# Optimization experiments

Measured on AMD Instinct MI355X. Metric: run time of the kernel, lower is better.

The kernel has to match this reference:

```python
import jax, jax.numpy as jnp
from jax import lax
import numpy as np

K = 3
PAD = (K - 1) // 2
EPS = 1e-5


def setup_inputs() -> dict:
    key = jax.random.key(0)
    k0, k1, k2, k3 = jax.random.split(key, 4)
    B, C, O, H, W = 8, 128, 128, 64, 64
    x = jax.random.normal(k0, (B, C, H, W), jnp.float32)
    bn_gamma = jnp.ones((C,), jnp.float32)
    bn_beta = jnp.zeros((C,), jnp.float32)
    bn_mean = jnp.zeros((C,), jnp.float32)
    bn_var = jnp.ones((C,), jnp.float32)
    # small offset-conv weights -> realistic sub-pixel offsets
    w_off = jax.random.normal(k1, (2 * K * K, C, K, K), jnp.float32) * 0.01
    b_off = jnp.zeros((2 * K * K,), jnp.float32)
    w_dconv = jax.random.normal(k2, (O, C, K, K), jnp.float32) * (1.0 / np.sqrt(C * K * K))
    b_dconv = jax.random.normal(k3, (O,), jnp.float32) * 0.01
    return dict(x=x, bn_gamma=bn_gamma, bn_beta=bn_beta, bn_mean=bn_mean,
                bn_var=bn_var, w_off=w_off, b_off=b_off,
                w_dconv=w_dconv, b_dconv=b_dconv)


def _conv2d(x, w, b):
    y = lax.conv_general_dilated(
        x, w, window_strides=(1, 1), padding=[(PAD, PAD), (PAD, PAD)],
        dimension_numbers=('NCHW', 'OIHW', 'NCHW'))
    return y + b[None, :, None, None]


def _deform_conv2d(x, offsets, w, b):
    # torchvision DeformConv2d semantics (deform_groups=1, groups=1, stride=1)
    B, C, H, W = x.shape
    KK = K * K
    off = offsets.reshape(B, KK, 2, H, W)  # (dy, dx) per kernel tap
    dy, dx = off[:, :, 0], off[:, :, 1]    # [B,KK,H,W]
    kh = (jnp.arange(KK) // K).astype(x.dtype)
    kw = (jnp.arange(KK) % K).astype(x.dtype)
    # sampling positions: p0 + pk - pad + offset
    py = dy + jnp.arange(H, dtype=x.dtype)[None, None, :, None] + (kh - PAD)[None, :, None, None]
    px = dx + jnp.arange(W, dtype=x.dtype)[None, None, None, :] + (kw - PAD)[None, :, None, None]
    y0 = jnp.floor(py)
    x0 = jnp.floor(px)
    wy = py - y0
    wx = px - x0
    y0i = y0.astype(jnp.int32)
    x0i = x0.astype(jnp.int32)
    xflat = x.reshape(B, C, H * W)

    def gather(yi, xi):
        valid = (yi >= 0) & (yi < H) & (xi >= 0) & (xi < W)
        idx = jnp.clip(yi, 0, H - 1) * W + jnp.clip(xi, 0, W - 1)  # [B,KK,H,W]
        vals = jax.vmap(lambda xf, ii: xf[:, ii])(xflat, idx)      # [B,C,KK,H,W]
        return vals * valid[:, None].astype(x.dtype)

    # bilinear sample with implicit zero padding outside the image
    v = (((1 - wy) * (1 - wx))[:, None] * gather(y0i, x0i)
         + ((1 - wy) * wx)[:, None] * gather(y0i, x0i + 1)
         + (wy * (1 - wx))[:, None] * gather(y0i + 1, x0i)
         + (wy * wx)[:, None] * gather(y0i + 1, x0i + 1))  # [B,C,KK,H,W]
    out = jnp.einsum('bckhw,ock->bohw', v, w.reshape(w.shape[0], C, KK))
    return out + b[None, :, None, None]


def reference(x, bn_gamma, bn_beta, bn_mean, bn_var, w_off, b_off, w_dconv, b_dconv):
    # BN (inference form) + ReLU
    inv = bn_gamma * lax.rsqrt(bn_var + EPS)
    h = jnp.maximum((x - bn_mean[None, :, None, None]) * inv[None, :, None, None]
                    + bn_beta[None, :, None, None], 0.0)
    offsets = _conv2d(h, w_off, b_off)          # [B, 2*K*K, H, W]
    return _deform_conv2d(h, offsets, w_dconv, b_dconv)
```

## Files before the change

kernel.cpp:

```cpp
#include <hip/hip_runtime.h>

#define BB 8
#define CC 128
#define OO 128
#define HH 64
#define WW 64
#define HW (HH*WW)

typedef __attribute__((ext_vector_type(8))) __bf16 bf16x8;
typedef __attribute__((ext_vector_type(4))) __bf16 bf16x4;
typedef __attribute__((ext_vector_type(4))) float  f32x4;

__global__ __launch_bounds__(256) void transform_weights(
    const float* __restrict__ w_dconv,
    const float* __restrict__ w_off,
    __bf16* __restrict__ wt_bf,
    __bf16* __restrict__ w_off_b)
{
    int idx = blockIdx.x * 256 + threadIdx.x;
    if (idx < 9 * 128 * 128) {
        int c  = idx & 127;
        int o  = (idx >> 7) & 127;
        int kk = idx >> 14;
        wt_bf[idx] = (__bf16)w_dconv[(o * 128 + c) * 9 + kk];
    }
    if (idx < 9 * 32 * 128) {
        int c  = idx & 127;
        int o  = (idx >> 7) & 31;
        int kk = idx >> 12;
        float v = (o < 18) ? w_off[o * 1152 + c * 9 + kk] : 0.f;
        w_off_b[idx] = (__bf16)v;
    }
}

__global__ __launch_bounds__(256) void bn_relu_nhwc(
    const float* __restrict__ x,
    const float* __restrict__ gamma, const float* __restrict__ beta,
    const float* __restrict__ mean,  const float* __restrict__ var,
    __bf16* __restrict__ h)
{
    __shared__ float inv_s[128], bb_s[128];
    __shared__ __bf16 tile[64 * 130];
    int blk = blockIdx.x;
    int b = blk & 7, y = blk >> 3;
    int tid = threadIdx.x;

    if (tid < 128) {
        float iv = gamma[tid] * rsqrtf(var[tid] + 1e-5f);
        inv_s[tid] = iv;
        bb_s[tid]  = beta[tid] - mean[tid] * iv;
    }
    __syncthreads();

    const float* xb = x + (size_t)b * CC * HW + (size_t)y * WW;
    #pragma unroll
    for (int i = 0; i < 8; ++i) {
        int idx = i * 256 + tid;
        int c = idx >> 4, x4 = idx & 15;
        float4 v = *(const float4*)(xb + (size_t)c * HW + x4 * 4);
        float iv = inv_s[c], bb = bb_s[c];
        tile[(x4 * 4 + 0) * 130 + c] = (__bf16)fmaxf(v.x * iv + bb, 0.f);
        tile[(x4 * 4 + 1) * 130 + c] = (__bf16)fmaxf(v.y * iv + bb, 0.f);
        tile[(x4 * 4 + 2) * 130 + c] = (__bf16)fmaxf(v.z * iv + bb, 0.f);
        tile[(x4 * 4 + 3) * 130 + c] = (__bf16)fmaxf(v.w * iv + bb, 0.f);
    }
    __syncthreads();

    __bf16* hb = h + ((size_t)b * HW + (size_t)y * WW) * CC;
    #pragma unroll
    for (int i = 0; i < 2; ++i) {
        int idx = i * 256 + tid;
        int xx = idx >> 3, c16 = idx & 7;
        const uint* src = (const uint*)&tile[xx * 130 + c16 * 16];
        uint r0 = src[0], r1 = src[1], r2 = src[2], r3 = src[3];
        uint r4 = src[4], r5 = src[5], r6 = src[6], r7 = src[7];
        uint* dst = (uint*)(hb + (size_t)xx * CC + c16 * 16);
        *(uint4*)dst       = (uint4){r0, r1, r2, r3};
        *(uint4*)(dst + 4) = (uint4){r4, r5, r6, r7};
    }
}

__global__ __launch_bounds__(256) void offset_mfma(
    const __bf16* __restrict__ h,
    const __bf16* __restrict__ w_off_b,
    const float* __restrict__ b_off,
    float* __restrict__ offs)
{
    __shared__ __align__(16) __bf16 at[64 * 136];
    __shared__ __align__(16) __bf16 bt[32 * 136];
    int blk = blockIdx.x;
    int b = blk & 7, y = blk >> 3;
    int tid = threadIdx.x;
    int lane = tid & 63;
    int wv  = __builtin_amdgcn_readfirstlane(tid >> 6);
    int l15 = lane & 15, quad = lane >> 4;

    const __bf16* hb = h + (size_t)b * HW * CC;

    f32x4 acc[2];
    acc[0] = (f32x4){0.f, 0.f, 0.f, 0.f};
    acc[1] = (f32x4){0.f, 0.f, 0.f, 0.f};

    for (int kk = 0; kk < 9; ++kk) {
        int dy = kk / 3 - 1, dx = kk % 3 - 1;
        int yy = y + dy;
        bool yok = (yy >= 0) && (yy < HH);
        __syncthreads();
        #pragma unroll
        for (int i = 0; i < 4; ++i) {
            int idx = i * 256 + tid;
            int xx = idx >> 4, c8 = idx & 15;
            int xs = xx + dx;
            uint4 v = (uint4){0u, 0u, 0u, 0u};
            if (yok && xs >= 0 && xs < WW)
                v = *(const uint4*)(hb + ((size_t)yy * WW + xs) * CC + c8 * 8);
            *(uint4*)&at[xx * 136 + c8 * 8] = v;
        }
        const __bf16* wsrc = w_off_b + (size_t)kk * 32 * 128;
        #pragma unroll
        for (int i = 0; i < 2; ++i) {
            int idx = i * 256 + tid;
            int o = idx >> 4, c8 = idx & 15;
            *(uint4*)&bt[o * 136 + c8 * 8] = *(const uint4*)(wsrc + o * 128 + c8 * 8);
        }
        __syncthreads();
        #pragma unroll
        for (int ks = 0; ks < 4; ++ks) {
            int kb = ks * 32 + quad * 8;
            bf16x8 a  = *(const bf16x8*)&at[(wv * 16 + l15) * 136 + kb];
            bf16x8 b0 = *(const bf16x8*)&bt[l15 * 136 + kb];
            bf16x8 b1 = *(const bf16x8*)&bt[(16 + l15) * 136 + kb];
            acc[0] = __builtin_amdgcn_mfma_f32_16x16x32_bf16(a, b0, acc[0], 0, 0, 0);
            acc[1] = __builtin_amdgcn_mfma_f32_16x16x32_bf16(a, b1, acc[1], 0, 0, 0);
        }
    }

    size_t ob = (size_t)b * 18 * HW + (size_t)y * WW;
    #pragma unroll
    for (int nt = 0; nt < 2; ++nt) {
        int oc = nt * 16 + l15;
        if (oc < 18) {
            float bias = b_off[oc];
            #pragma unroll
            for (int r = 0; r < 4; ++r) {
                int xx = wv * 16 + quad * 4 + r;
                offs[ob + (size_t)oc * HW + xx] = acc[nt][r] + bias;
            }
        }
    }
}

__global__ __launch_bounds__(256, 2) void deform_conv_mfma(
    const __bf16* __restrict__ h,
    const float* __restrict__ offs,
    const __bf16* __restrict__ wt,
    const float* __restrict__ b_dconv,
    float* __restrict__ out)
{
    __shared__ float pw[576 * 4];
    __shared__ int   pidx[576 * 4];
    __shared__ __align__(16) __bf16 vt[64 * 136];
    __shared__ __align__(16) __bf16 wl[128 * 136];

    int blk = blockIdx.x;
    int b = blk & 7, y = blk >> 3;
    int tid = threadIdx.x;

    const __bf16* hb = h + (size_t)b * HW * CC;
    size_t offbase = (size_t)b * 18 * HW + (size_t)y * WW;

    for (int e = tid; e < 576; e += 256) {
        int kk = e >> 6, xx = e & 63;
        float dy = offs[offbase + (size_t)(2 * kk) * HW + xx];
        float dx = offs[offbase + (size_t)(2 * kk + 1) * HW + xx];
        float py = dy + (float)y + (float)(kk / 3 - 1);
        float px = dx + (float)xx + (float)(kk % 3 - 1);
        float fy = floorf(py), fx = floorf(px);
        int y0 = (int)fy, x0 = (int)fx;
        float wy = py - fy, wx = px - fx;
        int y1 = y0 + 1, x1 = x0 + 1;
        bool vy0 = (y0 >= 0) && (y0 < HH);
        bool vy1 = (y1 >= 0) && (y1 < HH);
        bool vx0 = (x0 >= 0) && (x0 < WW);
        bool vx1 = (x1 >= 0) && (x1 < WW);
        int yc0 = min(max(y0, 0), HH - 1), yc1 = min(max(y1, 0), HH - 1);
        int xc0 = min(max(x0, 0), WW - 1), xc1 = min(max(x1, 0), WW - 1);
        pw[e * 4 + 0] = (vy0 && vx0) ? (1.f - wy) * (1.f - wx) : 0.f;
        pw[e * 4 + 1] = (vy0 && vx1) ? (1.f - wy) * wx         : 0.f;
        pw[e * 4 + 2] = (vy1 && vx0) ? wy * (1.f - wx)         : 0.f;
        pw[e * 4 + 3] = (vy1 && vx1) ? wy * wx                 : 0.f;
        pidx[e * 4 + 0] = (yc0 * WW + xc0) * CC;
        pidx[e * 4 + 1] = (yc0 * WW + xc1) * CC;
        pidx[e * 4 + 2] = (yc1 * WW + xc0) * CC;
        pidx[e * 4 + 3] = (yc1 * WW + xc1) * CC;
    }

    int lane = tid & 63;
    int wv   = __builtin_amdgcn_readfirstlane(tid >> 6);
    int l15  = lane & 15, quad = lane >> 4;
    int cl   = tid & 31, xh = tid >> 5;

    f32x4 acc[4][2];
    #pragma unroll
    for (int mt = 0; mt < 4; ++mt)
        #pragma unroll
        for (int nt = 0; nt < 2; ++nt)
            acc[mt][nt] = (f32x4){0.f, 0.f, 0.f, 0.f};

    for (int kk = 0; kk < 9; ++kk) {
        __syncthreads();
        const uint4* wsrc = (const uint4*)(wt + (size_t)kk * OO * CC);
        #pragma unroll
        for (int j = 0; j < 8; ++j) {
            int idx = j * 256 + tid;
            int cs = idx & 15, o = idx >> 4;
            *(uint4*)&wl[o * 136 + cs * 8] = wsrc[idx];
        }
        #pragma unroll
        for (int j = 0; j < 8; ++j) {
            int xx = xh * 8 + j;
            int e = (kk << 6) + xx;
            float w0 = pw[e * 4 + 0], w1 = pw[e * 4 + 1];
            float w2 = pw[e * 4 + 2], w3 = pw[e * 4 + 3];
            bf16x4 t0 = *(const bf16x4*)(hb + pidx[e * 4 + 0] + cl * 4);
            bf16x4 t1 = *(const bf16x4*)(hb + pidx[e * 4 + 1] + cl * 4);
            bf16x4 t2 = *(const bf16x4*)(hb + pidx[e * 4 + 2] + cl * 4);
            bf16x4 t3 = *(const bf16x4*)(hb + pidx[e * 4 + 3] + cl * 4);
            float rx = w0 * (float)t0[0] + w1 * (float)t1[0] + w2 * (float)t2[0] + w3 * (float)t3[0];
            float ry = w0 * (float)t0[1] + w1 * (float)t1[1] + w2 * (float)t2[1] + w3 * (float)t3[1];
            float rz = w0 * (float)t0[2] + w1 * (float)t1[2] + w2 * (float)t2[2] + w3 * (float)t3[2];
            float rw = w0 * (float)t0[3] + w1 * (float)t1[3] + w2 * (float)t2[3] + w3 * (float)t3[3];
            bf16x4 pk = {(__bf16)rx, (__bf16)ry, (__bf16)rz, (__bf16)rw};
            *(bf16x4*)&vt[xx * 136 + cl * 4] = pk;
        }
        __syncthreads();
        #pragma unroll
        for (int ks = 0; ks < 4; ++ks) {
            int kb = ks * 32 + quad * 8;
            bf16x8 a0 = *(const bf16x8*)&vt[(0 * 16 + l15) * 136 + kb];
            bf16x8 a1 = *(const bf16x8*)&vt[(1 * 16 + l15) * 136 + kb];
            bf16x8 a2 = *(const bf16x8*)&vt[(2 * 16 + l15) * 136 + kb];
            bf16x8 a3 = *(const bf16x8*)&vt[(3 * 16 + l15) * 136 + kb];
            bf16x8 b0 = *(const bf16x8*)&wl[(wv * 32 + l15) * 136 + kb];
            bf16x8 b1 = *(const bf16x8*)&wl[(wv * 32 + 16 + l15) * 136 + kb];
            acc[0][0] = __builtin_amdgcn_mfma_f32_16x16x32_bf16(a0, b0, acc[0][0], 0, 0, 0);
            acc[1][0] = __builtin_amdgcn_mfma_f32_16x16x32_bf16(a1, b0, acc[1][0], 0, 0, 0);
            acc[2][0] = __builtin_amdgcn_mfma_f32_16x16x32_bf16(a2, b0, acc[2][0], 0, 0, 0);
            acc[3][0] = __builtin_amdgcn_mfma_f32_16x16x32_bf16(a3, b0, acc[3][0], 0, 0, 0);
            acc[0][1] = __builtin_amdgcn_mfma_f32_16x16x32_bf16(a0, b1, acc[0][1], 0, 0, 0);
            acc[1][1] = __builtin_amdgcn_mfma_f32_16x16x32_bf16(a1, b1, acc[1][1], 0, 0, 0);
            acc[2][1] = __builtin_amdgcn_mfma_f32_16x16x32_bf16(a2, b1, acc[2][1], 0, 0, 0);
            acc[3][1] = __builtin_amdgcn_mfma_f32_16x16x32_bf16(a3, b1, acc[3][1], 0, 0, 0);
        }
    }

    size_t ob = (size_t)b * OO * HW + (size_t)y * WW;
    #pragma unroll
    for (int nt = 0; nt < 2; ++nt) {
        int o = wv * 32 + nt * 16 + l15;
        float bias = b_dconv[o];
        #pragma unroll
        for (int mt = 0; mt < 4; ++mt) {
            int xb = mt * 16 + quad * 4;
            float4 r;
            r.x = acc[mt][nt][0] + bias;
            r.y = acc[mt][nt][1] + bias;
            r.z = acc[mt][nt][2] + bias;
            r.w = acc[mt][nt][3] + bias;
            *(float4*)&out[ob + (size_t)o * HW + xb] = r;
        }
    }
}

extern "C" void kernel_launch(void* const* d_in, const int* in_sizes, int n_in,
                              void* d_out, int out_size, void* d_ws, size_t ws_size,
                              hipStream_t stream)
{
    const float* x       = (const float*)d_in[0];
    const float* gamma   = (const float*)d_in[1];
    const float* beta    = (const float*)d_in[2];
    const float* mean    = (const float*)d_in[3];
    const float* var     = (const float*)d_in[4];
    const float* w_off   = (const float*)d_in[5];
    const float* b_off   = (const float*)d_in[6];
    const float* w_dconv = (const float*)d_in[7];
    const float* b_dconv = (const float*)d_in[8];
    float* out = (float*)d_out;

    char* ws = (char*)d_ws;
    __bf16* h_bf    = (__bf16*)ws;
    float*  offs    = (float*)(ws + 8388608);
    __bf16* wt_bf   = (__bf16*)(ws + 10747904);
    __bf16* w_off_b = (__bf16*)(ws + 11042816);

    transform_weights<<<576, 256, 0, stream>>>(w_dconv, w_off, wt_bf, w_off_b);
    bn_relu_nhwc<<<512, 256, 0, stream>>>(x, gamma, beta, mean, var, h_bf);
    offset_mfma<<<512, 256, 0, stream>>>(h_bf, w_off_b, b_off, offs);
    deform_conv_mfma<<<512, 256, 0, stream>>>(h_bf, offs, wt_bf, b_dconv, out);
}
```

Measured before the change: 135.0 us.

## Fuse offset conv into deform conv kernel and read weights directly from global

Merges the offset-convolution kernel into the deformable-conv kernel, so each block computes its row's offsets in shared memory and no longer round-trips them through global memory or pays a separate launch. The shared-memory weight staging (wl and bt) is dropped, and MFMA B operands are loaded straight from global memory (L2/L1). This cuts LDS use enough to allow 4 blocks per CU. The cost is uncoalesced, per-wave repeated global weight loads inside the MFMA loop, which may add latency.

```diff
diff --git a/kernel.cpp b/kernel.cpp
--- a/kernel.cpp
+++ b/kernel.cpp
@@ -80,26 +80,32 @@
     }
 }
 
-__global__ __launch_bounds__(256) void offset_mfma(
+__global__ __launch_bounds__(256, 4) void fused_offset_deform(
     const __bf16* __restrict__ h,
     const __bf16* __restrict__ w_off_b,
     const float* __restrict__ b_off,
-    float* __restrict__ offs)
-{
-    __shared__ __align__(16) __bf16 at[64 * 136];
-    __shared__ __align__(16) __bf16 bt[32 * 136];
+    const __bf16* __restrict__ wt,
+    const float* __restrict__ b_dconv,
+    float* __restrict__ out)
+{
+    __shared__ float pw[576 * 4];
+    __shared__ int   pidx[576 * 4];
+    __shared__ __align__(16) __bf16 vt[64 * 136];
+    __shared__ float offs_s[18 * 65];
+
     int blk = blockIdx.x;
     int b = blk & 7, y = blk >> 3;
     int tid = threadIdx.x;
     int lane = tid & 63;
-    int wv  = __builtin_amdgcn_readfirstlane(tid >> 6);
-    int l15 = lane & 15, quad = lane >> 4;
+    int wv   = __builtin_amdgcn_readfirstlane(tid >> 6);
+    int l15  = lane & 15, quad = lane >> 4;
+    int cl   = tid & 31, xh = tid >> 5;
 
     const __bf16* hb = h + (size_t)b * HW * CC;
 
-    f32x4 acc[2];
-    acc[0] = (f32x4){0.f, 0.f, 0.f, 0.f};
-    acc[1] = (f32x4){0.f, 0.f, 0.f, 0.f};
+    f32x4 oacc[2];
+    oacc[0] = (f32x4){0.f, 0.f, 0.f, 0.f};
+    oacc[1] = (f32x4){0.f, 0.f, 0.f, 0.f};
 
     for (int kk = 0; kk < 9; ++kk) {
         int dy = kk / 3 - 1, dx = kk % 3 - 1;
@@ -114,28 +120,20 @@
             uint4 v = (uint4){0u, 0u, 0u, 0u};
             if (yok && xs >= 0 && xs < WW)
                 v = *(const uint4*)(hb + ((size_t)yy * WW + xs) * CC + c8 * 8);
-            *(uint4*)&at[xx * 136 + c8 * 8] = v;
-        }
-        const __bf16* wsrc = w_off_b + (size_t)kk * 32 * 128;
-        #pragma unroll
-        for (int i = 0; i < 2; ++i) {
-            int idx = i * 256 + tid;
-            int o = idx >> 4, c8 = idx & 15;
-            *(uint4*)&bt[o * 136 + c8 * 8] = *(const uint4*)(wsrc + o * 128 + c8 * 8);
-        }
-        __syncthreads();
+            *(uint4*)&vt[xx * 136 + c8 * 8] = v;
+        }
+        __syncthreads();
+        const __bf16* wk = w_off_b + (size_t)kk * 32 * 128;
         #pragma unroll
         for (int ks = 0; ks < 4; ++ks) {
             int kb = ks * 32 + quad * 8;
-            bf16x8 a  = *(const bf16x8*)&at[(wv * 16 + l15) * 136 + kb];
-            bf16x8 b0 = *(const bf16x8*)&bt[l15 * 136 + kb];
-            bf16x8 b1 = *(const bf16x8*)&bt[(16 + l15) * 136 + kb];
-            acc[0] = __builtin_amdgcn_mfma_f32_16x16x32_bf16(a, b0, acc[0], 0, 0, 0);
-            acc[1] = __builtin_amdgcn_mfma_f32_16x16x32_bf16(a, b1, acc[1], 0, 0, 0);
-        }
-    }
-
-    size_t ob = (size_t)b * 18 * HW + (size_t)y * WW;
+            bf16x8 a  = *(const bf16x8*)&vt[(wv * 16 + l15) * 136 + kb];
+            bf16x8 b0 = *(const bf16x8*)(wk + l15 * 128 + kb);
+            bf16x8 b1 = *(const bf16x8*)(wk + (16 + l15) * 128 + kb);
+            oacc[0] = __builtin_amdgcn_mfma_f32_16x16x32_bf16(a, b0, oacc[0], 0, 0, 0);
+            oacc[1] = __builtin_amdgcn_mfma_f32_16x16x32_bf16(a, b1, oacc[1], 0, 0, 0);
+        }
+    }
     #pragma unroll
     for (int nt = 0; nt < 2; ++nt) {
         int oc = nt * 16 + l15;
@@ -144,35 +142,16 @@
             #pragma unroll
             for (int r = 0; r < 4; ++r) {
                 int xx = wv * 16 + quad * 4 + r;
-                offs[ob + (size_t)oc * HW + xx] = acc[nt][r] + bias;
+                offs_s[oc * 65 + xx] = oacc[nt][r] + bias;
             }
         }
     }
-}
-
-__global__ __launch_bounds__(256, 2) void deform_conv_mfma(
-    const __bf16* __restrict__ h,
-    const float* __restrict__ offs,
-    const __bf16* __restrict__ wt,
-    const float* __restrict__ b_dconv,
-    float* __restrict__ out)
-{
-    __shared__ float pw[576 * 4];
-    __shared__ int   pidx[576 * 4];
-    __shared__ __align__(16) __bf16 vt[64 * 136];
-    __shared__ __align__(16) __bf16 wl[128 * 136];
-
-    int blk = blockIdx.x;
-    int b = blk & 7, y = blk >> 3;
-    int tid = threadIdx.x;
-
-    const __bf16* hb = h + (size_t)b * HW * CC;
-    size_t offbase = (size_t)b * 18 * HW + (size_t)y * WW;
+    __syncthreads();
 
     for (int e = tid; e < 576; e += 256) {
         int kk = e >> 6, xx = e & 63;
-        float dy = offs[offbase + (size_t)(2 * kk) * HW + xx];
-        float dx = offs[offbase + (size_t)(2 * kk + 1) * HW + xx];
+        float dy = offs_s[(2 * kk) * 65 + xx];
+        float dx = offs_s[(2 * kk + 1) * 65 + xx];
         float py = dy + (float)y + (float)(kk / 3 - 1);
         float px = dx + (float)xx + (float)(kk % 3 - 1);
         float fy = floorf(py), fx = floorf(px);
@@ -195,11 +174,6 @@
         pidx[e * 4 + 3] = (yc1 * WW + xc1) * CC;
     }
 
-    int lane = tid & 63;
-    int wv   = __builtin_amdgcn_readfirstlane(tid >> 6);
-    int l15  = lane & 15, quad = lane >> 4;
-    int cl   = tid & 31, xh = tid >> 5;
-
     f32x4 acc[4][2];
     #pragma unroll
     for (int mt = 0; mt < 4; ++mt)
@@ -209,13 +183,6 @@
 
     for (int kk = 0; kk < 9; ++kk) {
         __syncthreads();
-        const uint4* wsrc = (const uint4*)(wt + (size_t)kk * OO * CC);
-        #pragma unroll
-        for (int j = 0; j < 8; ++j) {
-            int idx = j * 256 + tid;
-            int cs = idx & 15, o = idx >> 4;
-            *(uint4*)&wl[o * 136 + cs * 8] = wsrc[idx];
-        }
         #pragma unroll
         for (int j = 0; j < 8; ++j) {
             int xx = xh * 8 + j;
@@ -234,15 +201,16 @@
             *(bf16x4*)&vt[xx * 136 + cl * 4] = pk;
         }
         __syncthreads();
+        const __bf16* wk = wt + (size_t)kk * OO * CC + (size_t)(wv * 32) * CC;
         #pragma unroll
         for (int ks = 0; ks < 4; ++ks) {
             int kb = ks * 32 + quad * 8;
+            bf16x8 b0 = *(const bf16x8*)(wk + l15 * CC + kb);
+            bf16x8 b1 = *(const bf16x8*)(wk + (16 + l15) * CC + kb);
             bf16x8 a0 = *(const bf16x8*)&vt[(0 * 16 + l15) * 136 + kb];
             bf16x8 a1 = *(const bf16x8*)&vt[(1 * 16 + l15) * 136 + kb];
             bf16x8 a2 = *(const bf16x8*)&vt[(2 * 16 + l15) * 136 + kb];
             bf16x8 a3 = *(const bf16x8*)&vt[(3 * 16 + l15) * 136 + kb];
-            bf16x8 b0 = *(const bf16x8*)&wl[(wv * 32 + l15) * 136 + kb];
-            bf16x8 b1 = *(const bf16x8*)&wl[(wv * 32 + 16 + l15) * 136 + kb];
             acc[0][0] = __builtin_amdgcn_mfma_f32_16x16x32_bf16(a0, b0, acc[0][0], 0, 0, 0);
             acc[1][0] = __builtin_amdgcn_mfma_f32_16x16x32_bf16(a1, b0, acc[1][0], 0, 0, 0);
             acc[2][0] = __builtin_amdgcn_mfma_f32_16x16x32_bf16(a2, b0, acc[2][0], 0, 0, 0);
@@ -289,12 +257,10 @@
 
     char* ws = (char*)d_ws;
     __bf16* h_bf    = (__bf16*)ws;
-    float*  offs    = (float*)(ws + 8388608);
-    __bf16* wt_bf   = (__bf16*)(ws + 10747904);
-    __bf16* w_off_b = (__bf16*)(ws + 11042816);
+    __bf16* wt_bf   = (__bf16*)(ws + 8388608);
+    __bf16* w_off_b = (__bf16*)(ws + 8683520);
 
     transform_weights<<<576, 256, 0, stream>>>(w_dconv, w_off, wt_bf, w_off_b);
     bn_relu_nhwc<<<512, 256, 0, stream>>>(x, gamma, beta, mean, var, h_bf);
-    offset_mfma<<<512, 256, 0, stream>>>(h_bf, w_off_b, b_off, offs);
-    deform_conv_mfma<<<512, 256, 0, stream>>>(h_bf, offs, wt_bf, b_dconv, out);
-}
+    fused_offset_deform<<<512, 256, 0, stream>>>(h_bf, w_off_b, b_off, wt_bf, b_dconv, out);
+}
```

Result: slower. 150.4 us (+11.4%).
